# Performance work log

Hardware: AMD Instinct MI355X
Metric: run time of the kernel (lower is better)

Reference implementation:

```python
import jax, jax.numpy as jnp
import numpy as np

DECAY = 0.95     # importance_decay
BUDGET = 1.0     # attention_budget
TOP_K = 10       # recall top_k used by get_context_embedding
EPS = 1e-8


def _gelu(x):
    # torch nn.GELU default = exact erf variant
    return jax.nn.gelu(x, approximate=False)


def setup_inputs() -> dict:
    key = jax.random.key(0)
    ks = jax.random.split(key, 8)
    B, N, D, H = 4096, 100, 4096, 128
    query = jax.random.normal(ks[0], (B, D), dtype=jnp.float32)
    seg_emb = jax.random.normal(ks[1], (N, D), dtype=jnp.float32)
    positions = jnp.arange(N, dtype=jnp.int32)
    s1 = 1.0 / np.sqrt(D)
    s2 = 1.0 / np.sqrt(H)
    iw1 = jax.random.normal(ks[2], (D, H), dtype=jnp.float32) * s1
    ib1 = jnp.zeros((H,), dtype=jnp.float32)
    iw2 = jax.random.normal(ks[3], (H, 1), dtype=jnp.float32) * s2
    ib2 = jnp.zeros((1,), dtype=jnp.float32)
    rw1 = jax.random.normal(ks[4], (2 * D, H), dtype=jnp.float32) * (1.0 / np.sqrt(2 * D))
    rb1 = jnp.zeros((H,), dtype=jnp.float32)
    rw2 = jax.random.normal(ks[5], (H, 1), dtype=jnp.float32) * s2
    rb2 = jnp.zeros((1,), dtype=jnp.float32)
    return {"query": query, "seg_emb": seg_emb, "positions": positions,
            "iw1": iw1, "ib1": ib1, "iw2": iw2, "ib2": ib2,
            "rw1": rw1, "rb1": rb1, "rw2": rw2, "rb2": rb2}


def reference(query, seg_emb, positions, iw1, ib1, iw2, ib2, rw1, rb1, rw2, rb2):
    # query: [B, D], seg_emb: [N, D]
    B, D = query.shape
    N = seg_emb.shape[0]

    # importance_scorer per segment: Linear->GELU->Linear->Sigmoid, [N]
    importance = jax.nn.sigmoid(_gelu(seg_emb @ iw1 + ib1) @ iw2 + ib2)[:, 0]

    # relevance_scorer on concat([query, seg]); split rw1 to avoid [B,N,2D] concat
    qh = query @ rw1[:D]            # [B, H]
    sh = seg_emb @ rw1[D:]          # [N, H]
    h = _gelu(qh[:, None, :] + sh[None, :, :] + rb1)   # [B, N, H]
    rel = jax.nn.sigmoid(jnp.einsum('bnh,ho->bn', h, rw2) + rb2[0])  # [B, N]

    # recall score: importance * relevance * (0.5 + 0.5 * decay^(N - pos - 1))
    pos_factor = DECAY ** (N - positions.astype(jnp.float32) - 1.0)  # [N]
    score = importance[None, :] * rel * (0.5 + 0.5 * pos_factor[None, :])

    _, topi = jax.lax.top_k(score, TOP_K)               # [B, K]

    sel_rel = jnp.take_along_axis(rel, topi, axis=1)    # [B, K]
    sel_imp = importance[topi]                          # [B, K]
    w = sel_imp * sel_rel
    w = w / (jnp.sum(w, axis=-1, keepdims=True) + EPS) * BUDGET

    sel_emb = seg_emb[topi]                             # [B, K, D]
    context = jnp.einsum('bk,bkd->bd', w, sel_emb)      # [B, D]
    return query + context
```

## Files before the change

### kernel.cpp

```cpp
#include <hip/hip_runtime.h>
#include <math.h>

#define DDIM 4096
#define NSEG 100
#define HDIM 128
#define BROWS 4096
#define TOPK 10
#define KSLICES 8

typedef __attribute__((ext_vector_type(8))) short bf16x8;
typedef __attribute__((ext_vector_type(4))) float f32x4;

__device__ __forceinline__ void gl16(const void* g, void* l) {
    __builtin_amdgcn_global_load_lds(
        (const __attribute__((address_space(1))) unsigned int*)g,
        (__attribute__((address_space(3))) unsigned int*)l,
        16, 0, 0);
}

__device__ __forceinline__ float gelu_f(float x) {
    float u  = x * 0.70710678118654752440f;
    float au = fminf(fabsf(u), 3.9f);
    float t  = __builtin_amdgcn_rcpf(fmaf(0.3275911f, au, 1.0f));
    float p  = fmaf(fmaf(fmaf(fmaf(1.061405429f, t, -1.453152027f), t,
                              1.421413741f), t, -0.284496736f), t, 0.254829592f) * t;
    float e  = __expf(-au * au);
    float er = fmaf(-p, e, 1.0f);
    er = copysignf(er, u);
    return 0.5f * x * (1.0f + er);
}

__device__ __forceinline__ void split8(const float4& a, const float4& b,
                                       bf16x8& hi, bf16x8& lo) {
    float v[8] = {a.x, a.y, a.z, a.w, b.x, b.y, b.z, b.w};
    uint hw[4], lw[4];
    #pragma unroll
    for (int j = 0; j < 4; ++j) {
        uint u0 = __float_as_uint(v[2 * j]);
        uint u1 = __float_as_uint(v[2 * j + 1]);
        hw[j] = (u0 >> 16) | (u1 & 0xffff0000u);
        float r0 = v[2 * j]     - __uint_as_float(u0 & 0xffff0000u);
        float r1 = v[2 * j + 1] - __uint_as_float(u1 & 0xffff0000u);
        lw[j] = (__float_as_uint(r0) >> 16) | (__float_as_uint(r1) & 0xffff0000u);
    }
    uint4 h = make_uint4(hw[0], hw[1], hw[2], hw[3]);
    uint4 l = make_uint4(lw[0], lw[1], lw[2], lw[3]);
    hi = __builtin_bit_cast(bf16x8, h);
    lo = __builtin_bit_cast(bf16x8, l);
}

__global__ void k_seg_gemm(const float* __restrict__ seg,
                           const float* __restrict__ iw1,
                           const float* __restrict__ rw1,
                           float* __restrict__ segp) {
    __shared__ float segT[64][5];
    int ng = blockIdx.x;
    int ks = blockIdx.y * 64;
    int tid = threadIdx.x;
    {
        int k = tid & 63, j = tid >> 6;
        segT[k][j] = seg[(size_t)(ng * 4 + j) * DDIM + ks + k];
    }
    __syncthreads();

    int col = tid;
    float a0 = 0.f, a1 = 0.f, a2 = 0.f, a3 = 0.f;
    const float* w = (col < HDIM) ? (iw1 + col)
                                  : (rw1 + (size_t)DDIM * HDIM + (col - HDIM));
    #pragma unroll 8
    for (int k = 0; k < 64; ++k) {
        float wv = w[(size_t)(ks + k) * HDIM];
        a0 = fmaf(segT[k][0], wv, a0);
        a1 = fmaf(segT[k][1], wv, a1);
        a2 = fmaf(segT[k][2], wv, a2);
        a3 = fmaf(segT[k][3], wv, a3);
    }
    float* outp = segp + (size_t)blockIdx.y * (NSEG * 256) + (size_t)(ng * 4) * 256 + col;
    outp[0] = a0; outp[256] = a1; outp[512] = a2; outp[768] = a3;
}

__global__ void k_seg_red(const float* __restrict__ segp,
                          const int* __restrict__ positions,
                          const float* __restrict__ ib1,
                          const float* __restrict__ iw2,
                          const float* __restrict__ ib2,
                          const float* __restrict__ rb1,
                          float* __restrict__ shwT, float* __restrict__ impA,
                          float* __restrict__ cA) {
    __shared__ float red[HDIM];
    int n = blockIdx.x, tid = threadIdx.x;
    float v = 0.f;
    #pragma unroll
    for (int s = 0; s < 64; ++s)
        v += segp[(size_t)s * (NSEG * 256) + (size_t)n * 256 + tid];
    if (tid < HDIM) {
        red[tid] = gelu_f(v + ib1[tid]) * iw2[tid];
    } else {
        shwT[(size_t)(tid - HDIM) * NSEG + n] = v + rb1[tid - HDIM];
    }
    __syncthreads();
    if (tid == 0) {
        float s = 0.f;
        for (int j = 0; j < HDIM; ++j) s += red[j];
        float imp = 1.f / (1.f + expf(-(s + ib2[0])));
        float pf = powf(0.95f, (float)NSEG - (float)positions[n] - 1.0f);
        impA[n] = imp;
        cA[n] = imp * (0.5f + 0.5f * pf);
    }
}

__global__ void k_bt(const float* __restrict__ rw1,
                     unsigned char* __restrict__ btI) {
    __shared__ float tile[32][129];
    int c = blockIdx.x, tid = threadIdx.x;
    #pragma unroll
    for (int i = 0; i < 4; ++i) {
        int e = i * 1024 + tid * 4;
        int k = e >> 7, n = e & 127;
        *reinterpret_cast<float4*>(&tile[k][n]) =
            *reinterpret_cast<const float4*>(rw1 + (size_t)(c * 32 + k) * HDIM + n);
    }
    __syncthreads();
    unsigned char* img = btI + (size_t)c * 16384;
    #pragma unroll
    for (int uu = 0; uu < 2; ++uu) {
        int U = tid * 2 + uu;
        int col = U >> 2;
        int u = U & 3;
        int Z = (col * 64 + u * 16) ^ ((col & 7) << 4);
        uint hw[4], lw[4];
        #pragma unroll
        for (int j = 0; j < 4; ++j) {
            float x0 = tile[u * 8 + 2 * j][col];
            float x1 = tile[u * 8 + 2 * j + 1][col];
            uint u0 = __float_as_uint(x0), u1 = __float_as_uint(x1);
            hw[j] = (u0 >> 16) | (u1 & 0xffff0000u);
            float r0 = x0 - __uint_as_float(u0 & 0xffff0000u);
            float r1 = x1 - __uint_as_float(u1 & 0xffff0000u);
            lw[j] = (__float_as_uint(r0) >> 16) | (__float_as_uint(r1) & 0xffff0000u);
        }
        *reinterpret_cast<uint4*>(img + Z)        = make_uint4(hw[0], hw[1], hw[2], hw[3]);
        *reinterpret_cast<uint4*>(img + 8192 + Z) = make_uint4(lw[0], lw[1], lw[2], lw[3]);
    }
}

__global__ __launch_bounds__(256)
void k_qh_mfma(const float* __restrict__ query,
               const unsigned char* __restrict__ btI,
               float* __restrict__ qhp) {
    __shared__ float  Ab[2][2048];
    __shared__ ushort Bb[2][8192];
    int tid = threadIdx.x;
    int lane = tid & 63, w = tid >> 6;
    int cl = lane & 15, rg = lane >> 4;
    int wm = w >> 1, wn = w & 1;
    int m0 = blockIdx.x * 64;
    int ky = blockIdx.y;
    int k0 = ky * 512;

    const float* aSrc0;
    const float* aSrc1;
    {
        int X0 = w * 2048 + lane * 16;
        int r0_ = X0 >> 7, kb0 = (X0 & 127) ^ ((r0_ & 7) << 4);
        aSrc0 = query + (size_t)(m0 + r0_) * DDIM + k0 + (kb0 >> 2);
        int X1 = X0 + 1024;
        int r1_ = X1 >> 7, kb1 = (X1 & 127) ^ ((r1_ & 7) << 4);
        aSrc1 = query + (size_t)(m0 + r1_) * DDIM + k0 + (kb1 >> 2);
    }
    const unsigned char* bSrc = btI + (size_t)(ky * 16) * 16384 + w * 4096 + lane * 16;

    f32x4 acc[2][4];
    #pragma unroll
    for (int mi = 0; mi < 2; ++mi)
        #pragma unroll
        for (int nf = 0; nf < 4; ++nf) acc[mi][nf] = (f32x4)0.f;

    {
        char* ad = (char*)&Ab[0][0] + w * 2048;
        char* bd = (char*)&Bb[0][0] + w * 4096;
        gl16(aSrc0, ad);
        gl16(aSrc1, ad + 1024);
        #pragma unroll
        for (int j = 0; j < 4; ++j) gl16(bSrc + j * 1024, bd + j * 1024);
    }
    __syncthreads();

    #pragma unroll 2
    for (int t = 0; t < 16; ++t) {
        int cur = t & 1;
        if (t < 15) {
            char* ad = (char*)&Ab[cur ^ 1][0] + w * 2048;
            char* bd = (char*)&Bb[cur ^ 1][0] + w * 4096;
            gl16(aSrc0 + (t + 1) * 32, ad);
            gl16(aSrc1 + (t + 1) * 32, ad + 1024);
            const unsigned char* bs = bSrc + (size_t)(t + 1) * 16384;
            #pragma unroll
            for (int j = 0; j < 4; ++j) gl16(bs + j * 1024, bd + j * 1024);
        }
        bf16x8 ah[2], al[2];
        #pragma unroll
        for (int mi = 0; mi < 2; ++mi) {
            int row = wm * 32 + mi * 16 + cl;
            int sw = (row & 7) << 4;
            int Sb = row * 128 + rg * 32;
            float4 f0 = *reinterpret_cast<const float4*>((const char*)&Ab[cur][0] + (Sb ^ sw));
            float4 f1 = *reinterpret_cast<const float4*>((const char*)&Ab[cur][0] + ((Sb + 16) ^ sw));
            split8(f0, f1, ah[mi], al[mi]);
        }
        #pragma unroll
        for (int nf = 0; nf < 4; ++nf) {
            int col = wn * 64 + nf * 16 + cl;
            int Z = (col * 64 + rg * 16) ^ ((col & 7) << 4);
            bf16x8 bh = *reinterpret_cast<const bf16x8*>((const char*)&Bb[cur][0] + Z);
            bf16x8 bl = *reinterpret_cast<const bf16x8*>((const char*)&Bb[cur][0] + 8192 + Z);
            #pragma unroll
            for (int mi = 0; mi < 2; ++mi) {
                acc[mi][nf] = __builtin_amdgcn_mfma_f32_16x16x32_bf16(ah[mi], bh, acc[mi][nf], 0, 0, 0);
                acc[mi][nf] = __builtin_amdgcn_mfma_f32_16x16x32_bf16(al[mi], bh, acc[mi][nf], 0, 0, 0);
                acc[mi][nf] = __builtin_amdgcn_mfma_f32_16x16x32_bf16(ah[mi], bl, acc[mi][nf], 0, 0, 0);
            }
        }
        __syncthreads();
    }

    float* op = qhp + (size_t)ky * (BROWS * HDIM);
    #pragma unroll
    for (int mi = 0; mi < 2; ++mi) {
        int rowb = m0 + wm * 32 + mi * 16 + rg * 4;
        #pragma unroll
        for (int nf = 0; nf < 4; ++nf) {
            int col = wn * 64 + nf * 16 + cl;
            #pragma unroll
            for (int r = 0; r < 4; ++r)
                op[(size_t)(rowb + r) * HDIM + col] = acc[mi][nf][r];
        }
    }
}

__global__ __launch_bounds__(256)
void k_rel(const float* __restrict__ qhp,
           const float* __restrict__ shwT,
           const float* __restrict__ rw2,
           const float* __restrict__ rb2,
           const float* __restrict__ impA,
           const float* __restrict__ cA,
           int* __restrict__ idxA,
           float* __restrict__ wnA) {
    __shared__ float qs[2][HDIM];
    __shared__ float scL[2][128], wiL[2][128];
    int tid = threadIdx.x;
    int b0 = blockIdx.x * 2;
    int g = tid >> 7, n = tid & 127;

    {
        size_t o = (size_t)(b0 + g) * HDIM + n;
        float v = qhp[o];
        #pragma unroll
        for (int s = 1; s < KSLICES; ++s)
            v += qhp[(size_t)s * (BROWS * HDIM) + o];
        qs[g][n] = v;
    }
    __syncthreads();

    int nn = (n < NSEG) ? n : (NSEG - 1);
    float a0 = 0.f;
    #pragma unroll 2
    for (int h = 0; h < HDIM; ++h) {
        float s = shwT[h * NSEG + nn];
        float w = rw2[h];
        a0 = fmaf(gelu_f(qs[g][h] + s), w, a0);
    }
    if (n < NSEG) {
        float rel = 1.f / (1.f + expf(-(a0 + rb2[0])));
        scL[g][n] = cA[n] * rel;
        wiL[g][n] = impA[n] * rel;
    }
    __syncthreads();

    int w = tid >> 6, lane = tid & 63;
    if (w < 2) {
        int rr = w;
        float s1 = scL[rr][lane];
        float w1 = wiL[rr][lane];
        int i2 = lane + 64;
        float s2 = (i2 < NSEG) ? scL[rr][i2] : -1e30f;
        float w2 = (i2 < NSEG) ? wiL[rr][i2] : 0.f;

        float wv[TOPK]; int idxv[TOPK]; float wsum = 0.f;
        #pragma unroll
        for (int k = 0; k < TOPK; ++k) {
            float s; int i;
            if (s2 > s1) { s = s2; i = i2; } else { s = s1; i = lane; }
            #pragma unroll
            for (int off = 1; off < 64; off <<= 1) {
                float os = __shfl_xor(s, off);
                int oi = __shfl_xor(i, off);
                if (os > s || (os == s && oi < i)) { s = os; i = oi; }
            }
            float wi = __shfl((i < 64) ? w1 : w2, i & 63);
            idxv[k] = i; wv[k] = wi; wsum += wi;
            if (i == lane) s1 = -1e30f;
            if (i == i2)   s2 = -1e30f;
        }
        if (lane == 0) {
            int b = b0 + rr;
            float denom = wsum + 1e-8f;
            #pragma unroll
            for (int k = 0; k < TOPK; ++k) {
                idxA[b * TOPK + k] = idxv[k];
                wnA[b * TOPK + k]  = wv[k] / denom;
            }
        }
    }
}

__global__ void k_gather(const float* __restrict__ query,
                         const float* __restrict__ seg,
                         const int* __restrict__ idxA,
                         const float* __restrict__ wnA,
                         float* __restrict__ out) {
    int b = blockIdx.x, tid = threadIdx.x;
    const int*   ip = idxA + b * TOPK;
    const float* wp = wnA  + b * TOPK;
    float wn[TOPK]; const float* srow[TOPK];
    #pragma unroll
    for (int k = 0; k < TOPK; ++k) {
        wn[k]   = wp[k];
        srow[k] = seg + (size_t)ip[k] * DDIM;
    }
    const float* qrow = query + (size_t)b * DDIM;
    float* orow = out + (size_t)b * DDIM;

    float4 q[4];
    #pragma unroll
    for (int c = 0; c < 4; ++c)
        q[c] = *reinterpret_cast<const float4*>(qrow + c * 1024 + tid * 4);
    #pragma unroll
    for (int k = 0; k < TOPK; ++k) {
        float4 s[4];
        #pragma unroll
        for (int c = 0; c < 4; ++c)
            s[c] = *reinterpret_cast<const float4*>(srow[k] + c * 1024 + tid * 4);
        #pragma unroll
        for (int c = 0; c < 4; ++c) {
            q[c].x = fmaf(wn[k], s[c].x, q[c].x);
            q[c].y = fmaf(wn[k], s[c].y, q[c].y);
            q[c].z = fmaf(wn[k], s[c].z, q[c].z);
            q[c].w = fmaf(wn[k], s[c].w, q[c].w);
        }
    }
    #pragma unroll
    for (int c = 0; c < 4; ++c)
        *reinterpret_cast<float4*>(orow + c * 1024 + tid * 4) = q[c];
}

extern "C" void kernel_launch(void* const* d_in, const int* in_sizes, int n_in,
                              void* d_out, int out_size, void* d_ws, size_t ws_size,
                              hipStream_t stream) {
    const float* query = (const float*)d_in[0];
    const float* seg   = (const float*)d_in[1];
    const int*   pos   = (const int*)d_in[2];
    const float* iw1   = (const float*)d_in[3];
    const float* ib1   = (const float*)d_in[4];
    const float* iw2   = (const float*)d_in[5];
    const float* ib2   = (const float*)d_in[6];
    const float* rw1   = (const float*)d_in[7];
    const float* rb1   = (const float*)d_in[8];
    const float* rw2   = (const float*)d_in[9];
    const float* rb2   = (const float*)d_in[10];
    float* out = (float*)d_out;

    char* ws = (char*)d_ws;
    float* qhp  = (float*)(ws);
    float* segp = (float*)(ws);
    unsigned char* btI = (unsigned char*)(ws + 16 * 1024 * 1024);
    float* shwT = (float*)(ws + 18 * 1024 * 1024);
    float* impA = (float*)(ws + 18 * 1024 * 1024 + 64 * 1024);
    float* cA   = (float*)(ws + 18 * 1024 * 1024 + 64 * 1024 + 4096);
    int*   idxA = (int*)  (ws + 18 * 1024 * 1024 + 128 * 1024);
    float* wnA  = (float*)(ws + 18 * 1024 * 1024 + 320 * 1024);

    hipLaunchKernelGGL(k_seg_gemm, dim3(25, 64), dim3(256), 0, stream, seg, iw1, rw1, segp);
    hipLaunchKernelGGL(k_seg_red, dim3(NSEG), dim3(256), 0, stream,
                       segp, pos, ib1, iw2, ib2, rb1, shwT, impA, cA);
    hipLaunchKernelGGL(k_bt, dim3(128), dim3(256), 0, stream, rw1, btI);
    hipLaunchKernelGGL(k_qh_mfma, dim3(64, KSLICES), dim3(256), 0, stream,
                       query, btI, qhp);
    hipLaunchKernelGGL(k_rel, dim3(BROWS / 2), dim3(256), 0, stream,
                       qhp, shwT, rw2, rb2, impA, cA, idxA, wnA);
    hipLaunchKernelGGL(k_gather, dim3(BROWS), dim3(256), 0, stream,
                       query, seg, idxA, wnA, out);
}
```

Measured before the change: 135.8 us.

## Merge six launches into three by co-scheduling independent stages and fusing gather

Independent stages now share launches through block-index branching: the segment GEMM and the weight split/transpose run as one front kernel, and the query MFMA GEMM runs alongside the segment reduction in a middle kernel. The top-k/relevance kernel now does the weighted gather and residual add itself, with indices and weights kept in shared memory. This removes launch gaps, tail effects, and the idx/weight round trip through global memory. The cost is a larger LDS footprint for the reduction blocks, and the gather now runs inside blocks that use more registers. The workspace layout changes so segp no longer aliases qhp, which is required now that they are live in the same kernel.

```diff
diff --git a/kernel.cpp b/kernel.cpp
--- a/kernel.cpp
+++ b/kernel.cpp
@@ -49,206 +49,211 @@
     lo = __builtin_bit_cast(bf16x8, l);
 }
 
-__global__ void k_seg_gemm(const float* __restrict__ seg,
-                           const float* __restrict__ iw1,
-                           const float* __restrict__ rw1,
-                           float* __restrict__ segp) {
-    __shared__ float segT[64][5];
-    int ng = blockIdx.x;
-    int ks = blockIdx.y * 64;
-    int tid = threadIdx.x;
-    {
-        int k = tid & 63, j = tid >> 6;
-        segT[k][j] = seg[(size_t)(ng * 4 + j) * DDIM + ks + k];
-    }
-    __syncthreads();
-
-    int col = tid;
-    float a0 = 0.f, a1 = 0.f, a2 = 0.f, a3 = 0.f;
-    const float* w = (col < HDIM) ? (iw1 + col)
-                                  : (rw1 + (size_t)DDIM * HDIM + (col - HDIM));
-    #pragma unroll 8
-    for (int k = 0; k < 64; ++k) {
-        float wv = w[(size_t)(ks + k) * HDIM];
-        a0 = fmaf(segT[k][0], wv, a0);
-        a1 = fmaf(segT[k][1], wv, a1);
-        a2 = fmaf(segT[k][2], wv, a2);
-        a3 = fmaf(segT[k][3], wv, a3);
-    }
-    float* outp = segp + (size_t)blockIdx.y * (NSEG * 256) + (size_t)(ng * 4) * 256 + col;
-    outp[0] = a0; outp[256] = a1; outp[512] = a2; outp[768] = a3;
-}
-
-__global__ void k_seg_red(const float* __restrict__ segp,
-                          const int* __restrict__ positions,
-                          const float* __restrict__ ib1,
-                          const float* __restrict__ iw2,
-                          const float* __restrict__ ib2,
-                          const float* __restrict__ rb1,
-                          float* __restrict__ shwT, float* __restrict__ impA,
-                          float* __restrict__ cA) {
-    __shared__ float red[HDIM];
-    int n = blockIdx.x, tid = threadIdx.x;
-    float v = 0.f;
-    #pragma unroll
-    for (int s = 0; s < 64; ++s)
-        v += segp[(size_t)s * (NSEG * 256) + (size_t)n * 256 + tid];
-    if (tid < HDIM) {
-        red[tid] = gelu_f(v + ib1[tid]) * iw2[tid];
+__global__ void k_front(const float* __restrict__ seg,
+                        const float* __restrict__ iw1,
+                        const float* __restrict__ rw1,
+                        float* __restrict__ segp,
+                        unsigned char* __restrict__ btI) {
+    __shared__ __align__(16) float shf[32 * 129];
+    int bid = blockIdx.x, tid = threadIdx.x;
+    if (bid < 1600) {
+        float (*segT)[5] = reinterpret_cast<float (*)[5]>(shf);
+        int ng = bid % 25;
+        int ks = (bid / 25) * 64;
+        {
+            int k = tid & 63, j = tid >> 6;
+            segT[k][j] = seg[(size_t)(ng * 4 + j) * DDIM + ks + k];
+        }
+        __syncthreads();
+        int col = tid;
+        float a0 = 0.f, a1 = 0.f, a2 = 0.f, a3 = 0.f;
+        const float* w = (col < HDIM) ? (iw1 + col)
+                                      : (rw1 + (size_t)DDIM * HDIM + (col - HDIM));
+        #pragma unroll 8
+        for (int k = 0; k < 64; ++k) {
+            float wv = w[(size_t)(ks + k) * HDIM];
+            a0 = fmaf(segT[k][0], wv, a0);
+            a1 = fmaf(segT[k][1], wv, a1);
+            a2 = fmaf(segT[k][2], wv, a2);
+            a3 = fmaf(segT[k][3], wv, a3);
+        }
+        float* outp = segp + (size_t)(bid / 25) * (NSEG * 256) + (size_t)(ng * 4) * 256 + col;
+        outp[0] = a0; outp[256] = a1; outp[512] = a2; outp[768] = a3;
     } else {
-        shwT[(size_t)(tid - HDIM) * NSEG + n] = v + rb1[tid - HDIM];
-    }
-    __syncthreads();
-    if (tid == 0) {
-        float s = 0.f;
-        for (int j = 0; j < HDIM; ++j) s += red[j];
-        float imp = 1.f / (1.f + expf(-(s + ib2[0])));
-        float pf = powf(0.95f, (float)NSEG - (float)positions[n] - 1.0f);
-        impA[n] = imp;
-        cA[n] = imp * (0.5f + 0.5f * pf);
-    }
-}
-
-__global__ void k_bt(const float* __restrict__ rw1,
-                     unsigned char* __restrict__ btI) {
-    __shared__ float tile[32][129];
-    int c = blockIdx.x, tid = threadIdx.x;
-    #pragma unroll
-    for (int i = 0; i < 4; ++i) {
-        int e = i * 1024 + tid * 4;
-        int k = e >> 7, n = e & 127;
-        *reinterpret_cast<float4*>(&tile[k][n]) =
-            *reinterpret_cast<const float4*>(rw1 + (size_t)(c * 32 + k) * HDIM + n);
-    }
-    __syncthreads();
-    unsigned char* img = btI + (size_t)c * 16384;
-    #pragma unroll
-    for (int uu = 0; uu < 2; ++uu) {
-        int U = tid * 2 + uu;
-        int col = U >> 2;
-        int u = U & 3;
-        int Z = (col * 64 + u * 16) ^ ((col & 7) << 4);
-        uint hw[4], lw[4];
-        #pragma unroll
-        for (int j = 0; j < 4; ++j) {
-            float x0 = tile[u * 8 + 2 * j][col];
-            float x1 = tile[u * 8 + 2 * j + 1][col];
-            uint u0 = __float_as_uint(x0), u1 = __float_as_uint(x1);
-            hw[j] = (u0 >> 16) | (u1 & 0xffff0000u);
-            float r0 = x0 - __uint_as_float(u0 & 0xffff0000u);
-            float r1 = x1 - __uint_as_float(u1 & 0xffff0000u);
-            lw[j] = (__float_as_uint(r0) >> 16) | (__float_as_uint(r1) & 0xffff0000u);
-        }
-        *reinterpret_cast<uint4*>(img + Z)        = make_uint4(hw[0], hw[1], hw[2], hw[3]);
-        *reinterpret_cast<uint4*>(img + 8192 + Z) = make_uint4(lw[0], lw[1], lw[2], lw[3]);
+        float (*tile)[129] = reinterpret_cast<float (*)[129]>(shf);
+        int c = bid - 1600;
+        #pragma unroll
+        for (int i = 0; i < 4; ++i) {
+            int e = i * 1024 + tid * 4;
+            int k = e >> 7, n = e & 127;
+            *reinterpret_cast<float4*>(&tile[k][n]) =
+                *reinterpret_cast<const float4*>(rw1 + (size_t)(c * 32 + k) * HDIM + n);
+        }
+        __syncthreads();
+        unsigned char* img = btI + (size_t)c * 16384;
+        #pragma unroll
+        for (int uu = 0; uu < 2; ++uu) {
+            int U = tid * 2 + uu;
+            int col = U >> 2;
+            int u = U & 3;
+            int Z = (col * 64 + u * 16) ^ ((col & 7) << 4);
+            uint hw[4], lw[4];
+            #pragma unroll
+            for (int j = 0; j < 4; ++j) {
+                float x0 = tile[u * 8 + 2 * j][col];
+                float x1 = tile[u * 8 + 2 * j + 1][col];
+                uint u0 = __float_as_uint(x0), u1 = __float_as_uint(x1);
+                hw[j] = (u0 >> 16) | (u1 & 0xffff0000u);
+                float r0 = x0 - __uint_as_float(u0 & 0xffff0000u);
+                float r1 = x1 - __uint_as_float(u1 & 0xffff0000u);
+                lw[j] = (__float_as_uint(r0) >> 16) | (__float_as_uint(r1) & 0xffff0000u);
+            }
+            *reinterpret_cast<uint4*>(img + Z)        = make_uint4(hw[0], hw[1], hw[2], hw[3]);
+            *reinterpret_cast<uint4*>(img + 8192 + Z) = make_uint4(lw[0], lw[1], lw[2], lw[3]);
+        }
     }
 }
 
 __global__ __launch_bounds__(256)
-void k_qh_mfma(const float* __restrict__ query,
-               const unsigned char* __restrict__ btI,
-               float* __restrict__ qhp) {
-    __shared__ float  Ab[2][2048];
-    __shared__ ushort Bb[2][8192];
-    int tid = threadIdx.x;
-    int lane = tid & 63, w = tid >> 6;
-    int cl = lane & 15, rg = lane >> 4;
-    int wm = w >> 1, wn = w & 1;
-    int m0 = blockIdx.x * 64;
-    int ky = blockIdx.y;
-    int k0 = ky * 512;
-
-    const float* aSrc0;
-    const float* aSrc1;
-    {
-        int X0 = w * 2048 + lane * 16;
-        int r0_ = X0 >> 7, kb0 = (X0 & 127) ^ ((r0_ & 7) << 4);
-        aSrc0 = query + (size_t)(m0 + r0_) * DDIM + k0 + (kb0 >> 2);
-        int X1 = X0 + 1024;
-        int r1_ = X1 >> 7, kb1 = (X1 & 127) ^ ((r1_ & 7) << 4);
-        aSrc1 = query + (size_t)(m0 + r1_) * DDIM + k0 + (kb1 >> 2);
-    }
-    const unsigned char* bSrc = btI + (size_t)(ky * 16) * 16384 + w * 4096 + lane * 16;
-
-    f32x4 acc[2][4];
-    #pragma unroll
-    for (int mi = 0; mi < 2; ++mi)
-        #pragma unroll
-        for (int nf = 0; nf < 4; ++nf) acc[mi][nf] = (f32x4)0.f;
-
-    {
-        char* ad = (char*)&Ab[0][0] + w * 2048;
-        char* bd = (char*)&Bb[0][0] + w * 4096;
-        gl16(aSrc0, ad);
-        gl16(aSrc1, ad + 1024);
-        #pragma unroll
-        for (int j = 0; j < 4; ++j) gl16(bSrc + j * 1024, bd + j * 1024);
-    }
-    __syncthreads();
-
-    #pragma unroll 2
-    for (int t = 0; t < 16; ++t) {
-        int cur = t & 1;
-        if (t < 15) {
-            char* ad = (char*)&Ab[cur ^ 1][0] + w * 2048;
-            char* bd = (char*)&Bb[cur ^ 1][0] + w * 4096;
-            gl16(aSrc0 + (t + 1) * 32, ad);
-            gl16(aSrc1 + (t + 1) * 32, ad + 1024);
-            const unsigned char* bs = bSrc + (size_t)(t + 1) * 16384;
-            #pragma unroll
-            for (int j = 0; j < 4; ++j) gl16(bs + j * 1024, bd + j * 1024);
-        }
-        bf16x8 ah[2], al[2];
+void k_mid(const float* __restrict__ query,
+           const unsigned char* __restrict__ btI,
+           float* __restrict__ qhp,
+           const float* __restrict__ segp,
+           const int* __restrict__ positions,
+           const float* __restrict__ ib1,
+           const float* __restrict__ iw2,
+           const float* __restrict__ ib2,
+           const float* __restrict__ rb1,
+           float* __restrict__ shwT, float* __restrict__ impA,
+           float* __restrict__ cA) {
+    __shared__ __align__(16) char lds[49152];
+    int bid = blockIdx.x, tid = threadIdx.x;
+    if (bid < 512) {
+        float  (*Ab)[2048] = reinterpret_cast<float (*)[2048]>(lds);
+        ushort (*Bb)[8192] = reinterpret_cast<ushort (*)[8192]>(lds + 16384);
+        int lane = tid & 63, w = tid >> 6;
+        int cl = lane & 15, rg = lane >> 4;
+        int wm = w >> 1, wn = w & 1;
+        int m0 = (bid & 63) * 64;
+        int ky = bid >> 6;
+        int k0 = ky * 512;
+
+        const float* aSrc0;
+        const float* aSrc1;
+        {
+            int X0 = w * 2048 + lane * 16;
+            int r0_ = X0 >> 7, kb0 = (X0 & 127) ^ ((r0_ & 7) << 4);
+            aSrc0 = query + (size_t)(m0 + r0_) * DDIM + k0 + (kb0 >> 2);
+            int X1 = X0 + 1024;
+            int r1_ = X1 >> 7, kb1 = (X1 & 127) ^ ((r1_ & 7) << 4);
+            aSrc1 = query + (size_t)(m0 + r1_) * DDIM + k0 + (kb1 >> 2);
+        }
+        const unsigned char* bSrc = btI + (size_t)(ky * 16) * 16384 + w * 4096 + lane * 16;
+
+        f32x4 acc[2][4];
+        #pragma unroll
+        for (int mi = 0; mi < 2; ++mi)
+            #pragma unroll
+            for (int nf = 0; nf < 4; ++nf) acc[mi][nf] = (f32x4)0.f;
+
+        {
+            char* ad = (char*)&Ab[0][0] + w * 2048;
+            char* bd = (char*)&Bb[0][0] + w * 4096;
+            gl16(aSrc0, ad);
+            gl16(aSrc1, ad + 1024);
+            #pragma unroll
+            for (int j = 0; j < 4; ++j) gl16(bSrc + j * 1024, bd + j * 1024);
+        }
+        __syncthreads();
+
+        #pragma unroll 2
+        for (int t = 0; t < 16; ++t) {
+            int cur = t & 1;
+            if (t < 15) {
+                char* ad = (char*)&Ab[cur ^ 1][0] + w * 2048;
+                char* bd = (char*)&Bb[cur ^ 1][0] + w * 4096;
+                gl16(aSrc0 + (t + 1) * 32, ad);
+                gl16(aSrc1 + (t + 1) * 32, ad + 1024);
+                const unsigned char* bs = bSrc + (size_t)(t + 1) * 16384;
+                #pragma unroll
+                for (int j = 0; j < 4; ++j) gl16(bs + j * 1024, bd + j * 1024);
+            }
+            bf16x8 ah[2], al[2];
+            #pragma unroll
+            for (int mi = 0; mi < 2; ++mi) {
+                int row = wm * 32 + mi * 16 + cl;
+                int sw = (row & 7) << 4;
+                int Sb = row * 128 + rg * 32;
+                float4 f0 = *reinterpret_cast<const float4*>((const char*)&Ab[cur][0] + (Sb ^ sw));
+                float4 f1 = *reinterpret_cast<const float4*>((const char*)&Ab[cur][0] + ((Sb + 16) ^ sw));
+                split8(f0, f1, ah[mi], al[mi]);
+            }
+            #pragma unroll
+            for (int nf = 0; nf < 4; ++nf) {
+                int col = wn * 64 + nf * 16 + cl;
+                int Z = (col * 64 + rg * 16) ^ ((col & 7) << 4);
+                bf16x8 bh = *reinterpret_cast<const bf16x8*>((const char*)&Bb[cur][0] + Z);
+                bf16x8 bl = *reinterpret_cast<const bf16x8*>((const char*)&Bb[cur][0] + 8192 + Z);
+                #pragma unroll
+                for (int mi = 0; mi < 2; ++mi) {
+                    acc[mi][nf] = __builtin_amdgcn_mfma_f32_16x16x32_bf16(ah[mi], bh, acc[mi][nf], 0, 0, 0);
+                    acc[mi][nf] = __builtin_amdgcn_mfma_f32_16x16x32_bf16(al[mi], bh, acc[mi][nf], 0, 0, 0);
+                    acc[mi][nf] = __builtin_amdgcn_mfma_f32_16x16x32_bf16(ah[mi], bl, acc[mi][nf], 0, 0, 0);
+                }
+            }
+            __syncthreads();
+        }
+
+        float* op = qhp + (size_t)ky * (BROWS * HDIM);
         #pragma unroll
         for (int mi = 0; mi < 2; ++mi) {
-            int row = wm * 32 + mi * 16 + cl;
-            int sw = (row & 7) << 4;
-            int Sb = row * 128 + rg * 32;
-            float4 f0 = *reinterpret_cast<const float4*>((const char*)&Ab[cur][0] + (Sb ^ sw));
-            float4 f1 = *reinterpret_cast<const float4*>((const char*)&Ab[cur][0] + ((Sb + 16) ^ sw));
-            split8(f0, f1, ah[mi], al[mi]);
-        }
-        #pragma unroll
-        for (int nf = 0; nf < 4; ++nf) {
-            int col = wn * 64 + nf * 16 + cl;
-            int Z = (col * 64 + rg * 16) ^ ((col & 7) << 4);
-            bf16x8 bh = *reinterpret_cast<const bf16x8*>((const char*)&Bb[cur][0] + Z);
-            bf16x8 bl = *reinterpret_cast<const bf16x8*>((const char*)&Bb[cur][0] + 8192 + Z);
-            #pragma unroll
-            for (int mi = 0; mi < 2; ++mi) {
-                acc[mi][nf] = __builtin_amdgcn_mfma_f32_16x16x32_bf16(ah[mi], bh, acc[mi][nf], 0, 0, 0);
-                acc[mi][nf] = __builtin_amdgcn_mfma_f32_16x16x32_bf16(al[mi], bh, acc[mi][nf], 0, 0, 0);
-                acc[mi][nf] = __builtin_amdgcn_mfma_f32_16x16x32_bf16(ah[mi], bl, acc[mi][nf], 0, 0, 0);
-            }
+            int rowb = m0 + wm * 32 + mi * 16 + rg * 4;
+            #pragma unroll
+            for (int nf = 0; nf < 4; ++nf) {
+                int col = wn * 64 + nf * 16 + cl;
+                #pragma unroll
+                for (int r = 0; r < 4; ++r)
+                    op[(size_t)(rowb + r) * HDIM + col] = acc[mi][nf][r];
+            }
+        }
+    } else {
+        float* red = reinterpret_cast<float*>(lds);
+        int n = bid - 512;
+        float v = 0.f;
+        #pragma unroll
+        for (int s = 0; s < 64; ++s)
+            v += segp[(size_t)s * (NSEG * 256) + (size_t)n * 256 + tid];
+        if (tid < HDIM) {
+            red[tid] = gelu_f(v + ib1[tid]) * iw2[tid];
+        } else {
+            shwT[(size_t)(tid - HDIM) * NSEG + n] = v + rb1[tid - HDIM];
         }
         __syncthreads();
-    }
-
-    float* op = qhp + (size_t)ky * (BROWS * HDIM);
-    #pragma unroll
-    for (int mi = 0; mi < 2; ++mi) {
-        int rowb = m0 + wm * 32 + mi * 16 + rg * 4;
-        #pragma unroll
-        for (int nf = 0; nf < 4; ++nf) {
-            int col = wn * 64 + nf * 16 + cl;
-            #pragma unroll
-            for (int r = 0; r < 4; ++r)
-                op[(size_t)(rowb + r) * HDIM + col] = acc[mi][nf][r];
+        if (tid == 0) {
+            float s = 0.f;
+            for (int j = 0; j < HDIM; ++j) s += red[j];
+            float imp = 1.f / (1.f + expf(-(s + ib2[0])));
+            float pf = powf(0.95f, (float)NSEG - (float)positions[n] - 1.0f);
+            impA[n] = imp;
+            cA[n] = imp * (0.5f + 0.5f * pf);
         }
     }
 }
 
 __global__ __launch_bounds__(256)
-void k_rel(const float* __restrict__ qhp,
-           const float* __restrict__ shwT,
-           const float* __restrict__ rw2,
-           const float* __restrict__ rb2,
-           const float* __restrict__ impA,
-           const float* __restrict__ cA,
-           int* __restrict__ idxA,
-           float* __restrict__ wnA) {
+void k_relg(const float* __restrict__ qhp,
+            const float* __restrict__ shwT,
+            const float* __restrict__ rw2,
+            const float* __restrict__ rb2,
+            const float* __restrict__ impA,
+            const float* __restrict__ cA,
+            const float* __restrict__ query,
+            const float* __restrict__ seg,
+            float* __restrict__ out) {
     __shared__ float qs[2][HDIM];
     __shared__ float scL[2][128], wiL[2][128];
+    __shared__ float wnS[2][TOPK];
+    __shared__ int   idxS[2][TOPK];
     int tid = threadIdx.x;
     int b0 = blockIdx.x * 2;
     int g = tid >> 7, n = tid & 127;
@@ -304,55 +309,42 @@
             if (i == i2)   s2 = -1e30f;
         }
         if (lane == 0) {
-            int b = b0 + rr;
             float denom = wsum + 1e-8f;
             #pragma unroll
             for (int k = 0; k < TOPK; ++k) {
-                idxA[b * TOPK + k] = idxv[k];
-                wnA[b * TOPK + k]  = wv[k] / denom;
-            }
-        }
-    }
-}
-
-__global__ void k_gather(const float* __restrict__ query,
-                         const float* __restrict__ seg,
-                         const int* __restrict__ idxA,
-                         const float* __restrict__ wnA,
-                         float* __restrict__ out) {
-    int b = blockIdx.x, tid = threadIdx.x;
-    const int*   ip = idxA + b * TOPK;
-    const float* wp = wnA  + b * TOPK;
-    float wn[TOPK]; const float* srow[TOPK];
+                idxS[rr][k] = idxv[k];
+                wnS[rr][k]  = wv[k] / denom;
+            }
+        }
+    }
+    __syncthreads();
+
     #pragma unroll
-    for (int k = 0; k < TOPK; ++k) {
-        wn[k]   = wp[k];
-        srow[k] = seg + (size_t)ip[k] * DDIM;
-    }
-    const float* qrow = query + (size_t)b * DDIM;
-    float* orow = out + (size_t)b * DDIM;
-
-    float4 q[4];
-    #pragma unroll
-    for (int c = 0; c < 4; ++c)
-        q[c] = *reinterpret_cast<const float4*>(qrow + c * 1024 + tid * 4);
-    #pragma unroll
-    for (int k = 0; k < TOPK; ++k) {
-        float4 s[4];
-        #pragma unroll
-        for (int c = 0; c < 4; ++c)
-            s[c] = *reinterpret_cast<const float4*>(srow[k] + c * 1024 + tid * 4);
+    for (int r = 0; r < 2; ++r) {
+        int b = b0 + r;
+        float wn_[TOPK]; const float* srow[TOPK];
+        #pragma unroll
+        for (int k = 0; k < TOPK; ++k) {
+            wn_[k]  = wnS[r][k];
+            srow[k] = seg + (size_t)idxS[r][k] * DDIM;
+        }
+        const float* qrow = query + (size_t)b * DDIM;
+        float* orow = out + (size_t)b * DDIM;
         #pragma unroll
         for (int c = 0; c < 4; ++c) {
-            q[c].x = fmaf(wn[k], s[c].x, q[c].x);
-            q[c].y = fmaf(wn[k], s[c].y, q[c].y);
-            q[c].z = fmaf(wn[k], s[c].z, q[c].z);
-            q[c].w = fmaf(wn[k], s[c].w, q[c].w);
-        }
-    }
-    #pragma unroll
-    for (int c = 0; c < 4; ++c)
-        *reinterpret_cast<float4*>(orow + c * 1024 + tid * 4) = q[c];
+            int d0 = c * 1024 + tid * 4;
+            float4 q4 = *reinterpret_cast<const float4*>(qrow + d0);
+            #pragma unroll
+            for (int k = 0; k < TOPK; ++k) {
+                float4 s4 = *reinterpret_cast<const float4*>(srow[k] + d0);
+                q4.x = fmaf(wn_[k], s4.x, q4.x);
+                q4.y = fmaf(wn_[k], s4.y, q4.y);
+                q4.z = fmaf(wn_[k], s4.z, q4.z);
+                q4.w = fmaf(wn_[k], s4.w, q4.w);
+            }
+            *reinterpret_cast<float4*>(orow + d0) = q4;
+        }
+    }
 }
 
 extern "C" void kernel_launch(void* const* d_in, const int* in_sizes, int n_in,
@@ -373,22 +365,17 @@
 
     char* ws = (char*)d_ws;
     float* qhp  = (float*)(ws);
-    float* segp = (float*)(ws);
-    unsigned char* btI = (unsigned char*)(ws + 16 * 1024 * 1024);
-    float* shwT = (float*)(ws + 18 * 1024 * 1024);
-    float* impA = (float*)(ws + 18 * 1024 * 1024 + 64 * 1024);
-    float* cA   = (float*)(ws + 18 * 1024 * 1024 + 64 * 1024 + 4096);
-    int*   idxA = (int*)  (ws + 18 * 1024 * 1024 + 128 * 1024);
-    float* wnA  = (float*)(ws + 18 * 1024 * 1024 + 320 * 1024);
-
-    hipLaunchKernelGGL(k_seg_gemm, dim3(25, 64), dim3(256), 0, stream, seg, iw1, rw1, segp);
-    hipLaunchKernelGGL(k_seg_red, dim3(NSEG), dim3(256), 0, stream,
-                       segp, pos, ib1, iw2, ib2, rb1, shwT, impA, cA);
-    hipLaunchKernelGGL(k_bt, dim3(128), dim3(256), 0, stream, rw1, btI);
-    hipLaunchKernelGGL(k_qh_mfma, dim3(64, KSLICES), dim3(256), 0, stream,
-                       query, btI, qhp);
-    hipLaunchKernelGGL(k_rel, dim3(BROWS / 2), dim3(256), 0, stream,
-                       qhp, shwT, rw2, rb2, impA, cA, idxA, wnA);
-    hipLaunchKernelGGL(k_gather, dim3(BROWS), dim3(256), 0, stream,
-                       query, seg, idxA, wnA, out);
-}
+    float* segp = (float*)(ws + 16 * 1024 * 1024);
+    unsigned char* btI = (unsigned char*)(ws + 23 * 1024 * 1024);
+    float* shwT = (float*)(ws + 25 * 1024 * 1024);
+    float* impA = (float*)(ws + 25 * 1024 * 1024 + 64 * 1024);
+    float* cA   = (float*)(ws + 25 * 1024 * 1024 + 64 * 1024 + 4096);
+
+    hipLaunchKernelGGL(k_front, dim3(1728), dim3(256), 0, stream,
+                       seg, iw1, rw1, segp, btI);
+    hipLaunchKernelGGL(k_mid, dim3(612), dim3(256), 0, stream,
+                       query, btI, qhp, segp, pos, ib1, iw2, ib2, rb1,
+                       shwT, impA, cA);
+    hipLaunchKernelGGL(k_relg, dim3(BROWS / 2), dim3(256), 0, stream,
+                       qhp, shwT, rw2, rb2, impA, cA, query, seg, out);
+}
```

Result: faster. 125.0 us (-7.9%).
